# Kernel optimization log

Hardware: AMD Instinct MI355X
Metric: run time of the kernel (lower is better)

## Reference

```python
import jax, jax.numpy as jnp
import numpy as np


def setup_inputs() -> dict:
    key = jax.random.key(0)
    ks = jax.random.split(key, 9)
    B, C, H, W = 4, 256, 128, 128
    d = C // 8
    x = jax.random.normal(ks[0], (B, C, H, W), jnp.float32)
    wq = jax.random.normal(ks[1], (d, C), jnp.float32) * 0.05
    bq = jax.random.normal(ks[2], (d,), jnp.float32) * 0.05
    wk = jax.random.normal(ks[3], (d, C), jnp.float32) * 0.05
    bk = jax.random.normal(ks[4], (d,), jnp.float32) * 0.05
    wv = jax.random.normal(ks[5], (d, C), jnp.float32) * 0.05
    bv = jax.random.normal(ks[6], (d,), jnp.float32) * 0.05
    wp = jax.random.normal(ks[7], (C, d, 3, 3), jnp.float32) * 0.05
    gamma = jax.random.normal(ks[8], (1,), jnp.float32)
    return dict(x=x, wq=wq, bq=bq, wk=wk, bk=bk, wv=wv, bv=bv, wp=wp, gamma=gamma)


def reference(x, wq, bq, wk, bk, wv, bv, wp, gamma):
    B, C, H, W = x.shape
    d = wq.shape[0]  # C // 8
    N = H * W
    # 1x1 convs expressed as channel matmuls
    q = jnp.einsum('bchw,dc->bdhw', x, wq) + bq[None, :, None, None]
    k = jnp.einsum('bchw,dc->bdhw', x, wk) + bk[None, :, None, None]
    v = jnp.einsum('bchw,dc->bdhw', x, wv) + bv[None, :, None, None]
    Q = q.reshape(B, d, N)
    K = k.reshape(B, d, N)
    V = v.reshape(B, d, N)
    # channel-channel energy: [B, d, d]
    energy = jnp.einsum('bdn,ben->bde', Q, K)
    energy_new = jnp.max(energy, axis=-1, keepdims=True) - energy
    attention = jax.nn.softmax(energy_new, axis=-1)
    out = jnp.einsum('bde,ben->bdn', attention, V).reshape(B, d, H, W)
    # 3x3 conv (no bias) + exact GELU
    out = jax.lax.conv_general_dilated(
        out, wp, window_strides=(1, 1), padding='SAME',
        dimension_numbers=('NCHW', 'OIHW', 'NCHW'))
    out = jax.nn.gelu(out, approximate=False)
    return gamma[0] * out + x
```

## Files before the change

kernel.cpp:

```cpp
#include <hip/hip_runtime.h>
#include <hip/hip_bf16.h>
#include <math.h>

#define BB 4
#define CC 256
#define HH 128
#define WW 128
#define NN (HH*WW)
#define DD 32

#define AOT_CI   44
#define AOT_ROWE (130*AOT_CI)
#define AOT_IMGE (130*AOT_ROWE)
#define AOT_BYTES ((size_t)BB*AOT_IMGE*2)
#define AOT_ALLOC (AOT_BYTES + 1024)

#define WT_BYTES (9*256*AOT_CI*2)

#define PATCH1   34320
#define WSLAB    22528
#define CONV_LDS1 (PATCH1 + 2*WSLAB)
#define EPI1_PITCH 132

#define ASWZ_BYTES 98304
#define QKVP 260
#define QKV_LDS 131584

typedef __attribute__((ext_vector_type(8)))  short bf16x8;
typedef __attribute__((ext_vector_type(4)))  float f32x4;
typedef __attribute__((ext_vector_type(16))) float f32x16;

__device__ inline void async_copy16(void* lds, const void* g) {
    __builtin_amdgcn_global_load_lds(
        (const __attribute__((address_space(1))) unsigned int*)g,
        (__attribute__((address_space(3))) unsigned int*)lds, 16, 0, 0);
}

__device__ inline unsigned short f2bf(float f) {
    __hip_bfloat16 h = __float2bfloat16(f);
    return *reinterpret_cast<unsigned short*>(&h);
}

__device__ inline void split2(float v, unsigned short& h, unsigned short& l) {
    __hip_bfloat16 hb = __float2bfloat16(v);
    float r = v - __bfloat162float(hb);
    __hip_bfloat16 lb = __float2bfloat16(r);
    h = *reinterpret_cast<unsigned short*>(&hb);
    l = *reinterpret_cast<unsigned short*>(&lb);
}

__device__ inline unsigned int packsplit(float v) {
    unsigned int fb = __float_as_uint(v);
    unsigned int hb = fb & 0xFFFF0000u;
    float r = v - __uint_as_float(hb);
    unsigned int lb = __float_as_uint(r) >> 16;
    return (hb >> 16) | (lb << 16);
}

__device__ inline bf16x8 ld_frag8(const char* p) {
    union { bf16x8 v; short4 h[2]; } u;
    u.h[0] = *(const short4*)(p);
    u.h[1] = *(const short4*)(p + 8);
    return u.v;
}

__device__ inline float gelu_fast(float v) {
    float a = fabsf(v) * 0.70710678118654752f;
    float t = __fdividef(1.0f, fmaf(0.3275911f, a, 1.0f));
    float p = t * fmaf(t, fmaf(t, fmaf(t, fmaf(t, 1.061405429f, -1.453152027f),
                                       1.421413741f), -0.284496736f), 0.254829592f);
    float e = 1.0f - p * __expf(-a * a);
    float erfv = (v < 0.0f) ? -e : e;
    return 0.5f * v * (1.0f + erfv);
}

__global__ __launch_bounds__(256) void prep_kernel(
    const float* __restrict__ wp, unsigned short* __restrict__ Wt,
    const float* __restrict__ wq, const float* __restrict__ wk,
    const float* __restrict__ wv, unsigned short* __restrict__ Aswz,
    unsigned short* __restrict__ AOT)
{
    const int blk = blockIdx.x;
    if (blk < 288) {
        int i = blk*256 + threadIdx.x;
        int kk = i / (256*32);
        int r  = i % (256*32);
        int co = r >> 5, ci = r & 31;
        float v = wp[((size_t)co*32 + ci)*9 + kk];
        Wt[((size_t)kk*256 + co)*AOT_CI + ci] = f2bf(v);
    } else if (blk < 480) {
        int i = (blk-288)*256 + threadIdx.x;
        int j    = i & 7;
        int lane = (i >> 3) & 63;
        int q9   = i >> 9;
        int cf   = q9 % 3;
        int t    = q9 / 3;
        int hl   = t & 1;
        int s    = t >> 1;
        int row  = cf*32 + (lane & 31);
        int c    = s*16 + (lane >> 5)*8 + j;
        float w  = (row < 32) ? wq[row*256 + c]
                 : (row < 64) ? wk[(row-32)*256 + c]
                              : wv[(row-64)*256 + c];
        unsigned short h, l;
        split2(w, h, l);
        Aswz[i] = hl ? l : h;
    } else {
        int idx = (blk-480)*256 + threadIdx.x;
        if (idx < BB*22704) {
            int b = idx / 22704;
            int r = idx % 22704;
            size_t off;
            if (r < 11440) {
                int row = (r < 5720) ? 0 : 129;
                int e   = (r < 5720) ? r : r - 5720;
                off = (size_t)b*AOT_IMGE + (size_t)row*AOT_ROWE + e;
            } else {
                int r2 = r - 11440;
                int rr = r2 / 88 + 1;
                int w2 = r2 % 88;
                int col = (w2 < 44) ? 0 : 129;
                int ci  = (w2 < 44) ? w2 : w2 - 44;
                off = (size_t)b*AOT_IMGE + (size_t)rr*AOT_ROWE
                    + (size_t)col*AOT_CI + ci;
            }
            AOT[off] = 0;
        }
    }
}

__global__ __launch_bounds__(512, 1) void qkv_mfma_kernel(
    const float* __restrict__ x, const unsigned short* __restrict__ Aswz,
    const float* __restrict__ bq, const float* __restrict__ bk,
    const float* __restrict__ bv,
    float* __restrict__ Vout, float* __restrict__ Ep)
{
    __shared__ __align__(16) char lds[QKV_LDS];
    const int b    = blockIdx.y;
    const int s    = blockIdx.x;
    const int n0   = s * 256;
    const int tid  = threadIdx.x;
    const int w    = tid >> 6;
    const int lane = tid & 63;
    const int l31  = lane & 31;
    const int lh   = lane >> 5;
    const int chl  = lane >> 3;
    const int nq   = lane & 7;

    for (int i = tid; i < 6144; i += 512)
        async_copy16(lds + i*16, (const char*)Aswz + i*16);
    float* biasL = (float*)(lds + 131072);
    if (tid < 96)
        biasL[tid] = (tid < 32) ? bq[tid] : (tid < 64) ? bk[tid-32] : bv[tid-64];

    char* mybuf = lds + 98304 + w*4096;
    const float* xq4 = x + (size_t)b*CC*NN + n0 + 32*w + nq*4;

    f32x16 acc0 = {0}, acc1 = {0}, acc2 = {0};

    float4 sa0, sb0, sa1, sb1, sa2, sb2;
    #define LOADX(VA, VB, R) do { \
        VA = *(const float4*)(xq4 + (size_t)((R)*16 + chl    )*NN); \
        VB = *(const float4*)(xq4 + (size_t)((R)*16 + 8 + chl)*NN); } while (0)
    #define PACKW(R, VA, VB) do { \
        unsigned int* bp = (unsigned int*)(mybuf + ((R) & 1)*2048); \
        uint4 ua, ub; \
        ua.x = packsplit((VA).x); ua.y = packsplit((VA).y); \
        ua.z = packsplit((VA).z); ua.w = packsplit((VA).w); \
        ub.x = packsplit((VB).x); ub.y = packsplit((VB).y); \
        ub.z = packsplit((VB).z); ub.w = packsplit((VB).w); \
        *(uint4*)(bp + (chl    )*32 + nq*4) = ua; \
        *(uint4*)(bp + (8 + chl)*32 + nq*4) = ub; } while (0)

    LOADX(sa0, sb0, 0);
    LOADX(sa1, sb1, 1);
    LOADX(sa2, sb2, 2);
    PACKW(0, sa0, sb0);
    __syncthreads();

    #pragma unroll
    for (int r = 0; r < 16; ++r) {
        if (r + 3 < 16) {
            if ((r+3) % 3 == 0)      LOADX(sa0, sb0, r+3);
            else if ((r+3) % 3 == 1) LOADX(sa1, sb1, r+3);
            else                     LOADX(sa2, sb2, r+3);
        }
        {
            const unsigned int* bufc = (const unsigned int*)(mybuf + (r & 1)*2048);
            unsigned int u[8];
            #pragma unroll
            for (int j = 0; j < 8; ++j)
                u[j] = bufc[(lh*8 + j)*32 + l31];
            union { bf16x8 v; unsigned int d[4]; } B1, B2;
            #pragma unroll
            for (int dq = 0; dq < 4; ++dq) {
                B1.d[dq] = (u[2*dq] & 0xFFFFu) | (u[2*dq+1] << 16);
                B2.d[dq] = (u[2*dq] >> 16)     | (u[2*dq+1] & 0xFFFF0000u);
            }
            #pragma unroll
            for (int cf = 0; cf < 3; ++cf) {
                bf16x8 ah = *(const bf16x8*)(lds + (((r*6 +     cf)*64) + lane)*16);
                bf16x8 al = *(const bf16x8*)(lds + (((r*6 + 3 + cf)*64) + lane)*16);
                f32x16* ac = (cf == 0) ? &acc0 : (cf == 1) ? &acc1 : &acc2;
                *ac = __builtin_amdgcn_mfma_f32_32x32x16_bf16(ah, B1.v, *ac, 0, 0, 0);
                *ac = __builtin_amdgcn_mfma_f32_32x32x16_bf16(ah, B2.v, *ac, 0, 0, 0);
                *ac = __builtin_amdgcn_mfma_f32_32x32x16_bf16(al, B1.v, *ac, 0, 0, 0);
                *ac = __builtin_amdgcn_mfma_f32_32x32x16_bf16(al, B2.v, *ac, 0, 0, 0);
            }
        }
        if (r + 1 < 16) {
            if ((r+1) % 3 == 0)      PACKW(r+1, sa0, sb0);
            else if ((r+1) % 3 == 1) PACKW(r+1, sa1, sb1);
            else                     PACKW(r+1, sa2, sb2);
        }
    }
    #undef LOADX
    #undef PACKW

    __syncthreads();
    float* qk = (float*)lds;
    #pragma unroll
    for (int r = 0; r < 16; ++r) {
        const int rsub = (r & 3) + 8*(r >> 2) + 4*lh;
        const int col  = 32*w + l31;
        qk[rsub*QKVP + col]      = acc0[r] + biasL[rsub];
        qk[(32+rsub)*QKVP + col] = acc1[r] + biasL[32 + rsub];
        Vout[((size_t)b*DD + rsub)*NN + n0 + col] = acc2[r] + biasL[64 + rsub];
    }
    __syncthreads();

    const int d  = tid >> 4;
    const int e2 = tid & 15;
    const float* qrow = qk + d*QKVP;
    float s0 = 0.f, s1 = 0.f;
    for (int n4 = 0; n4 < 256; n4 += 4) {
        float4 qv = *(const float4*)(qrow + n4);
        float4 ka = *(const float4*)(qk + (32 + e2)*QKVP + n4);
        float4 kb = *(const float4*)(qk + (48 + e2)*QKVP + n4);
        s0 += qv.x*ka.x + qv.y*ka.y + qv.z*ka.z + qv.w*ka.w;
        s1 += qv.x*kb.x + qv.y*kb.y + qv.z*kb.z + qv.w*kb.w;
    }
    float* ep = Ep + ((size_t)s*BB + b)*1024;
    ep[d*32 + e2]      = s0;
    ep[d*32 + e2 + 16] = s1;
}

__global__ __launch_bounds__(256) void pv_kernel(
    const float* __restrict__ V, const float* __restrict__ Ep,
    unsigned short* __restrict__ AOT)
{
    __shared__ float Vs[DD][256];
    __shared__ float at4[DD][DD];
    const int b  = blockIdx.y;
    const int n0 = blockIdx.x * 256;
    const int tid = threadIdx.x;
    for (int i = tid; i < 2048; i += 256) {
        int r = i >> 6, c4 = i & 63;
        *(float4*)&Vs[r][c4*4] =
            *(const float4*)(V + ((size_t)b*DD + r)*NN + n0 + c4*4);
    }
    {
        const int d  = tid >> 3;
        const int eb = (tid & 7) * 4;
        float4 sum = {0.f, 0.f, 0.f, 0.f};
        #pragma unroll 8
        for (int p = 0; p < 64; ++p) {
            float4 v = *(const float4*)(Ep + ((size_t)p*BB + b)*1024 + d*32 + eb);
            sum.x += v.x; sum.y += v.y; sum.z += v.z; sum.w += v.w;
        }
        float nv0 = -sum.x, nv1 = -sum.y, nv2 = -sum.z, nv3 = -sum.w;
        float m = fmaxf(fmaxf(nv0, nv1), fmaxf(nv2, nv3));
        m = fmaxf(m, __shfl_xor(m, 4, 8));
        m = fmaxf(m, __shfl_xor(m, 2, 8));
        m = fmaxf(m, __shfl_xor(m, 1, 8));
        float p0 = expf(nv0 - m), p1 = expf(nv1 - m);
        float p2 = expf(nv2 - m), p3 = expf(nv3 - m);
        float su = p0 + p1 + p2 + p3;
        su += __shfl_xor(su, 4, 8);
        su += __shfl_xor(su, 2, 8);
        su += __shfl_xor(su, 1, 8);
        const float inv = 1.0f / su;
        at4[eb + 0][d] = p0 * inv;
        at4[eb + 1][d] = p1 * inv;
        at4[eb + 2][d] = p2 * inv;
        at4[eb + 3][d] = p3 * inv;
    }
    __syncthreads();

    const int t = tid;
    float acc[DD];
    #pragma unroll
    for (int k = 0; k < DD; ++k) acc[k] = 0.f;
    #pragma unroll 4
    for (int e = 0; e < DD; ++e) {
        float v = Vs[e][t];
        const float4* ar = (const float4*)at4[e];
        #pragma unroll
        for (int dq = 0; dq < 8; ++dq) {
            float4 a = ar[dq];
            acc[4*dq+0] += a.x * v; acc[4*dq+1] += a.y * v;
            acc[4*dq+2] += a.z * v; acc[4*dq+3] += a.w * v;
        }
    }
    const int n = n0 + t;
    const int h = n >> 7, ww = n & 127;
    unsigned short* dst = AOT + (size_t)b*AOT_IMGE + (size_t)(h+1)*AOT_ROWE
                              + (size_t)(ww+1)*AOT_CI;
    #pragma unroll
    for (int q = 0; q < 8; ++q) {
        ushort4 u;
        u.x = f2bf(acc[4*q+0]); u.y = f2bf(acc[4*q+1]);
        u.z = f2bf(acc[4*q+2]); u.w = f2bf(acc[4*q+3]);
        *(ushort4*)(dst + 4*q) = u;
    }
}

__global__ __launch_bounds__(256, 2) void conv_kernel(
    const unsigned short* __restrict__ AOT, const unsigned short* __restrict__ Wt,
    const float* __restrict__ gammap, const float* __restrict__ x,
    float* __restrict__ out)
{
    __shared__ __align__(16) char lds[CONV_LDS1];
    const int b   = blockIdx.y;
    const int h   = blockIdx.x;
    const int tid = threadIdx.x;
    const int wid = tid >> 6;
    const int lane = tid & 63;
    const int l15 = lane & 15;
    const int lj  = lane >> 4;

    const char* psrc = (const char*)(AOT + (size_t)b*AOT_IMGE + (size_t)h*AOT_ROWE);
    for (int i = tid; i < PATCH1/16; i += 256)
        async_copy16(lds + i*16, psrc + i*16);
    for (int i = tid; i < WSLAB/16; i += 256)
        async_copy16(lds + PATCH1 + i*16, (const char*)Wt + i*16);
    __syncthreads();

    f32x4 acc[4][8];
    #pragma unroll
    for (int cf = 0; cf < 4; ++cf)
        #pragma unroll
        for (int nf = 0; nf < 8; ++nf)
            acc[cf][nf] = (f32x4){0.f, 0.f, 0.f, 0.f};

    for (int kk = 0; kk < 9; ++kk) {
        if (kk < 8) {
            const char* wsrc = (const char*)Wt + (size_t)(kk+1)*WSLAB;
            char* wdst = lds + PATCH1 + ((kk+1)&1)*WSLAB;
            for (int i = tid; i < WSLAB/16; i += 256)
                async_copy16(wdst + i*16, wsrc + i*16);
        }
        const int kh = kk / 3, kw = kk % 3;
        const char* wbase = lds + PATCH1 + (kk&1)*WSLAB;
        bf16x8 af[4];
        #pragma unroll
        for (int cf = 0; cf < 4; ++cf)
            af[cf] = ld_frag8(wbase + (wid*64 + cf*16 + l15)*88 + lj*16);
        #pragma unroll
        for (int nf = 0; nf < 8; ++nf) {
            const int cell = kh*130 + nf*16 + l15 + kw;
            const bf16x8 bfr = ld_frag8(lds + cell*88 + lj*16);
            #pragma unroll
            for (int cf = 0; cf < 4; ++cf)
                acc[cf][nf] = __builtin_amdgcn_mfma_f32_16x16x32_bf16(
                    af[cf], bfr, acc[cf][nf], 0, 0, 0);
        }
        __syncthreads();
    }

    const float g0 = gammap[0];
    float* lf = (float*)lds;
    for (int k = 0; k < 4; ++k) {
        if (wid == k) {
            #pragma unroll
            for (int cf = 0; cf < 4; ++cf) {
                const int rl = cf*16 + 4*lj;
                #pragma unroll
                for (int nf = 0; nf < 8; ++nf) {
                    const int col = nf*16 + l15;
                    #pragma unroll
                    for (int j = 0; j < 4; ++j)
                        lf[(rl + j)*EPI1_PITCH + col] = acc[cf][nf][j];
                }
            }
        }
        __syncthreads();
        #pragma unroll
        for (int it = 0; it < 8; ++it) {
            const int idx = tid + it*256;
            const int row = idx >> 5, c4 = idx & 31;
            const int co  = k*64 + row;
            const size_t g = ((size_t)b*CC + co)*NN + (size_t)h*WW + c4*4;
            float4 v  = *(const float4*)(lf + row*EPI1_PITCH + c4*4);
            float4 xv = *(const float4*)(x + g);
            float4 o;
            o.x = g0*gelu_fast(v.x) + xv.x;
            o.y = g0*gelu_fast(v.y) + xv.y;
            o.z = g0*gelu_fast(v.z) + xv.z;
            o.w = g0*gelu_fast(v.w) + xv.w;
            *(float4*)(out + g) = o;
        }
        __syncthreads();
    }
}

extern "C" void kernel_launch(void* const* d_in, const int* in_sizes, int n_in,
                              void* d_out, int out_size, void* d_ws, size_t ws_size,
                              hipStream_t stream)
{
    const float* x  = (const float*)d_in[0];
    const float* wq = (const float*)d_in[1];
    const float* bq = (const float*)d_in[2];
    const float* wk = (const float*)d_in[3];
    const float* bk = (const float*)d_in[4];
    const float* wv = (const float*)d_in[5];
    const float* bv = (const float*)d_in[6];
    const float* wp = (const float*)d_in[7];
    const float* gm = (const float*)d_in[8];
    float* out = (float*)d_out;

    float* Vbuf = out;

    char* ws = (char*)d_ws;
    unsigned short* AOT  = (unsigned short*)ws;
    unsigned short* Wt   = (unsigned short*)(ws + AOT_ALLOC);
    unsigned short* Aswz = (unsigned short*)(ws + AOT_ALLOC + WT_BYTES);
    float* Ep  = (float*)(ws + AOT_ALLOC + WT_BYTES + ASWZ_BYTES);

    prep_kernel    <<<dim3(835), 256, 0, stream>>>(wp, Wt, wq, wk, wv, Aswz, AOT);
    qkv_mfma_kernel<<<dim3(64, BB), 512, 0, stream>>>(x, Aswz, bq, bk, bv, Vbuf, Ep);
    pv_kernel      <<<dim3(64, BB), 256, 0, stream>>>(Vbuf, Ep, AOT);
    conv_kernel    <<<dim3(HH, BB), 256, 0, stream>>>(AOT, Wt, gm, x, out);
}
```

Before: 75.75 us.

## Shrink QKV blocks to 128 columns and stream weight fragments from global

Result: slower. 79.43 us (+4.9%).

```diff
diff --git a/kernel.cpp b/kernel.cpp
--- a/kernel.cpp
+++ b/kernel.cpp
@@ -23,8 +23,8 @@
 #define EPI1_PITCH 132
 
 #define ASWZ_BYTES 98304
-#define QKVP 260
-#define QKV_LDS 131584
+#define QKV8_PITCH 132
+#define QKV8_LDS   34304
 
 typedef __attribute__((ext_vector_type(8)))  short bf16x8;
 typedef __attribute__((ext_vector_type(4)))  float f32x4;
@@ -129,16 +129,16 @@
     }
 }
 
-__global__ __launch_bounds__(512, 1) void qkv_mfma_kernel(
+__global__ __launch_bounds__(256, 3) void qkv_mfma_kernel(
     const float* __restrict__ x, const unsigned short* __restrict__ Aswz,
     const float* __restrict__ bq, const float* __restrict__ bk,
     const float* __restrict__ bv,
     float* __restrict__ Vout, float* __restrict__ Ep)
 {
-    __shared__ __align__(16) char lds[QKV_LDS];
+    __shared__ __align__(16) char lds[QKV8_LDS];
     const int b    = blockIdx.y;
     const int s    = blockIdx.x;
-    const int n0   = s * 256;
+    const int n0   = s * 128;
     const int tid  = threadIdx.x;
     const int w    = tid >> 6;
     const int lane = tid & 63;
@@ -147,21 +147,28 @@
     const int chl  = lane >> 3;
     const int nq   = lane & 7;
 
-    for (int i = tid; i < 6144; i += 512)
-        async_copy16(lds + i*16, (const char*)Aswz + i*16);
-    float* biasL = (float*)(lds + 131072);
+    float* biasL = (float*)(lds + 33792);
     if (tid < 96)
         biasL[tid] = (tid < 32) ? bq[tid] : (tid < 64) ? bk[tid-32] : bv[tid-64];
 
-    char* mybuf = lds + 98304 + w*4096;
+    char* mybuf = lds + w*4096;
     const float* xq4 = x + (size_t)b*CC*NN + n0 + 32*w + nq*4;
+    const bf16x8* Ab = (const bf16x8*)Aswz;
 
     f32x16 acc0 = {0}, acc1 = {0}, acc2 = {0};
 
     float4 sa0, sb0, sa1, sb1, sa2, sb2;
+    bf16x8 aqA[6], aqB[6];
     #define LOADX(VA, VB, R) do { \
         VA = *(const float4*)(xq4 + (size_t)((R)*16 + chl    )*NN); \
         VB = *(const float4*)(xq4 + (size_t)((R)*16 + 8 + chl)*NN); } while (0)
+    #define LOADA(Q, R) do { \
+        Q[0] = Ab[(((R)*2+0)*3 + 0)*64 + lane]; \
+        Q[1] = Ab[(((R)*2+0)*3 + 1)*64 + lane]; \
+        Q[2] = Ab[(((R)*2+0)*3 + 2)*64 + lane]; \
+        Q[3] = Ab[(((R)*2+1)*3 + 0)*64 + lane]; \
+        Q[4] = Ab[(((R)*2+1)*3 + 1)*64 + lane]; \
+        Q[5] = Ab[(((R)*2+1)*3 + 2)*64 + lane]; } while (0)
     #define PACKW(R, VA, VB) do { \
         unsigned int* bp = (unsigned int*)(mybuf + ((R) & 1)*2048); \
         uint4 ua, ub; \
@@ -171,12 +178,38 @@
         ub.z = packsplit((VB).z); ub.w = packsplit((VB).w); \
         *(uint4*)(bp + (chl    )*32 + nq*4) = ua; \
         *(uint4*)(bp + (8 + chl)*32 + nq*4) = ub; } while (0)
+    #define COMPUTE(R, AQ) do { \
+        const unsigned int* bufc = (const unsigned int*)(mybuf + ((R) & 1)*2048); \
+        unsigned int u[8]; \
+        _Pragma("unroll") \
+        for (int j = 0; j < 8; ++j) \
+            u[j] = bufc[(lh*8 + j)*32 + l31]; \
+        union { bf16x8 v; unsigned int d[4]; } B1, B2; \
+        _Pragma("unroll") \
+        for (int dq = 0; dq < 4; ++dq) { \
+            B1.d[dq] = (u[2*dq] & 0xFFFFu) | (u[2*dq+1] << 16); \
+            B2.d[dq] = (u[2*dq] >> 16)     | (u[2*dq+1] & 0xFFFF0000u); \
+        } \
+        acc0 = __builtin_amdgcn_mfma_f32_32x32x16_bf16(AQ[0], B1.v, acc0, 0, 0, 0); \
+        acc1 = __builtin_amdgcn_mfma_f32_32x32x16_bf16(AQ[1], B1.v, acc1, 0, 0, 0); \
+        acc2 = __builtin_amdgcn_mfma_f32_32x32x16_bf16(AQ[2], B1.v, acc2, 0, 0, 0); \
+        acc0 = __builtin_amdgcn_mfma_f32_32x32x16_bf16(AQ[3], B2.v, acc0, 0, 0, 0); \
+        acc1 = __builtin_amdgcn_mfma_f32_32x32x16_bf16(AQ[4], B2.v, acc1, 0, 0, 0); \
+        acc2 = __builtin_amdgcn_mfma_f32_32x32x16_bf16(AQ[5], B2.v, acc2, 0, 0, 0); \
+        acc0 = __builtin_amdgcn_mfma_f32_32x32x16_bf16(AQ[3], B1.v, acc0, 0, 0, 0); \
+        acc1 = __builtin_amdgcn_mfma_f32_32x32x16_bf16(AQ[4], B1.v, acc1, 0, 0, 0); \
+        acc2 = __builtin_amdgcn_mfma_f32_32x32x16_bf16(AQ[5], B1.v, acc2, 0, 0, 0); \
+        acc0 = __builtin_amdgcn_mfma_f32_32x32x16_bf16(AQ[0], B2.v, acc0, 0, 0, 0); \
+        acc1 = __builtin_amdgcn_mfma_f32_32x32x16_bf16(AQ[1], B2.v, acc1, 0, 0, 0); \
+        acc2 = __builtin_amdgcn_mfma_f32_32x32x16_bf16(AQ[2], B2.v, acc2, 0, 0, 0); \
+    } while (0)
 
     LOADX(sa0, sb0, 0);
     LOADX(sa1, sb1, 1);
     LOADX(sa2, sb2, 2);
+    LOADA(aqA, 0);
+    LOADA(aqB, 1);
     PACKW(0, sa0, sb0);
-    __syncthreads();
 
     #pragma unroll
     for (int r = 0; r < 16; ++r) {
@@ -185,28 +218,12 @@
             else if ((r+3) % 3 == 1) LOADX(sa1, sb1, r+3);
             else                     LOADX(sa2, sb2, r+3);
         }
-        {
-            const unsigned int* bufc = (const unsigned int*)(mybuf + (r & 1)*2048);
-            unsigned int u[8];
-            #pragma unroll
-            for (int j = 0; j < 8; ++j)
-                u[j] = bufc[(lh*8 + j)*32 + l31];
-            union { bf16x8 v; unsigned int d[4]; } B1, B2;
-            #pragma unroll
-            for (int dq = 0; dq < 4; ++dq) {
-                B1.d[dq] = (u[2*dq] & 0xFFFFu) | (u[2*dq+1] << 16);
-                B2.d[dq] = (u[2*dq] >> 16)     | (u[2*dq+1] & 0xFFFF0000u);
-            }
-            #pragma unroll
-            for (int cf = 0; cf < 3; ++cf) {
-                bf16x8 ah = *(const bf16x8*)(lds + (((r*6 +     cf)*64) + lane)*16);
-                bf16x8 al = *(const bf16x8*)(lds + (((r*6 + 3 + cf)*64) + lane)*16);
-                f32x16* ac = (cf == 0) ? &acc0 : (cf == 1) ? &acc1 : &acc2;
-                *ac = __builtin_amdgcn_mfma_f32_32x32x16_bf16(ah, B1.v, *ac, 0, 0, 0);
-                *ac = __builtin_amdgcn_mfma_f32_32x32x16_bf16(ah, B2.v, *ac, 0, 0, 0);
-                *ac = __builtin_amdgcn_mfma_f32_32x32x16_bf16(al, B1.v, *ac, 0, 0, 0);
-                *ac = __builtin_amdgcn_mfma_f32_32x32x16_bf16(al, B2.v, *ac, 0, 0, 0);
-            }
+        if ((r & 1) == 0) {
+            COMPUTE(r, aqA);
+            if (r + 2 < 16) LOADA(aqA, r+2);
+        } else {
+            COMPUTE(r, aqB);
+            if (r + 2 < 16) LOADA(aqB, r+2);
         }
         if (r + 1 < 16) {
             if ((r+1) % 3 == 0)      PACKW(r+1, sa0, sb0);
@@ -215,7 +232,9 @@
         }
     }
     #undef LOADX
+    #undef LOADA
     #undef PACKW
+    #undef COMPUTE
 
     __syncthreads();
     float* qk = (float*)lds;
@@ -223,26 +242,33 @@
     for (int r = 0; r < 16; ++r) {
         const int rsub = (r & 3) + 8*(r >> 2) + 4*lh;
         const int col  = 32*w + l31;
-        qk[rsub*QKVP + col]      = acc0[r] + biasL[rsub];
-        qk[(32+rsub)*QKVP + col] = acc1[r] + biasL[32 + rsub];
+        qk[rsub*QKV8_PITCH + col]      = acc0[r] + biasL[rsub];
+        qk[(32+rsub)*QKV8_PITCH + col] = acc1[r] + biasL[32 + rsub];
         Vout[((size_t)b*DD + rsub)*NN + n0 + col] = acc2[r] + biasL[64 + rsub];
     }
     __syncthreads();
 
-    const int d  = tid >> 4;
-    const int e2 = tid & 15;
-    const float* qrow = qk + d*QKVP;
-    float s0 = 0.f, s1 = 0.f;
-    for (int n4 = 0; n4 < 256; n4 += 4) {
+    const int d  = tid >> 3;
+    const int e0 = tid & 7;
+    const float* qrow = qk + d*QKV8_PITCH;
+    float s0 = 0.f, s1 = 0.f, s2 = 0.f, s3 = 0.f;
+    #pragma unroll 4
+    for (int n4 = 0; n4 < 128; n4 += 4) {
         float4 qv = *(const float4*)(qrow + n4);
-        float4 ka = *(const float4*)(qk + (32 + e2)*QKVP + n4);
-        float4 kb = *(const float4*)(qk + (48 + e2)*QKVP + n4);
-        s0 += qv.x*ka.x + qv.y*ka.y + qv.z*ka.z + qv.w*ka.w;
-        s1 += qv.x*kb.x + qv.y*kb.y + qv.z*kb.z + qv.w*kb.w;
+        float4 k0 = *(const float4*)(qk + (32 + e0     )*QKV8_PITCH + n4);
+        float4 k1 = *(const float4*)(qk + (32 + e0 +  8)*QKV8_PITCH + n4);
+        float4 k2 = *(const float4*)(qk + (32 + e0 + 16)*QKV8_PITCH + n4);
+        float4 k3 = *(const float4*)(qk + (32 + e0 + 24)*QKV8_PITCH + n4);
+        s0 += qv.x*k0.x + qv.y*k0.y + qv.z*k0.z + qv.w*k0.w;
+        s1 += qv.x*k1.x + qv.y*k1.y + qv.z*k1.z + qv.w*k1.w;
+        s2 += qv.x*k2.x + qv.y*k2.y + qv.z*k2.z + qv.w*k2.w;
+        s3 += qv.x*k3.x + qv.y*k3.y + qv.z*k3.z + qv.w*k3.w;
     }
     float* ep = Ep + ((size_t)s*BB + b)*1024;
-    ep[d*32 + e2]      = s0;
-    ep[d*32 + e2 + 16] = s1;
+    ep[d*32 + e0]      = s0;
+    ep[d*32 + e0 + 8]  = s1;
+    ep[d*32 + e0 + 16] = s2;
+    ep[d*32 + e0 + 24] = s3;
 }
 
 __global__ __launch_bounds__(256) void pv_kernel(
@@ -264,7 +290,7 @@
         const int eb = (tid & 7) * 4;
         float4 sum = {0.f, 0.f, 0.f, 0.f};
         #pragma unroll 8
-        for (int p = 0; p < 64; ++p) {
+        for (int p = 0; p < 128; ++p) {
             float4 v = *(const float4*)(Ep + ((size_t)p*BB + b)*1024 + d*32 + eb);
             sum.x += v.x; sum.y += v.y; sum.z += v.z; sum.w += v.w;
         }
@@ -428,7 +454,7 @@
     float* Ep  = (float*)(ws + AOT_ALLOC + WT_BYTES + ASWZ_BYTES);
 
     prep_kernel    <<<dim3(835), 256, 0, stream>>>(wp, Wt, wq, wk, wv, Aswz, AOT);
-    qkv_mfma_kernel<<<dim3(64, BB), 512, 0, stream>>>(x, Aswz, bq, bk, bv, Vbuf, Ep);
+    qkv_mfma_kernel<<<dim3(128, BB), 256, 0, stream>>>(x, Aswz, bq, bk, bv, Vbuf, Ep);
     pv_kernel      <<<dim3(64, BB), 256, 0, stream>>>(Vbuf, Ep, AOT);
     conv_kernel    <<<dim3(HH, BB), 256, 0, stream>>>(AOT, Wt, gm, x, out);
 }
```
